# Kernel tuning notes

Hardware: AMD Instinct MI355X
Metric: run time of the kernel (lower is better)

The kernel has to match this reference:

```python
import jax, jax.numpy as jnp
import numpy as np

KEEP_RATIO = 0.5
B, H, W = 8, 1024, 1024


def setup_inputs() -> dict:
    key = jax.random.key(0)
    k1, k2, k3 = jax.random.split(key, 3)
    logits = jax.random.normal(k1, (B, 1, H, W), dtype=jnp.float32)
    targets = jax.random.randint(k2, (B, 1, H, W), 0, 2, dtype=jnp.int32)
    tissue_mask = jax.random.randint(k3, (B, 1, H, W), 0, 2, dtype=jnp.int32)
    return {"logits": logits, "targets": targets, "tissue_mask": tissue_mask}


def reference(logits, targets, tissue_mask):
    b = logits.shape[0]
    x = logits.reshape(b, -1)                       # (B, N)
    t = targets.reshape(b, -1).astype(x.dtype)      # {0,1}
    m = tissue_mask.reshape(b, -1).astype(x.dtype)  # {0,1}
    n = x.shape[1]

    # stable binary_cross_entropy_with_logits, reduction='none'
    bce = jnp.maximum(x, 0.0) - x * t + jnp.log1p(jnp.exp(-jnp.abs(x)))
    loss = bce * m                                  # masked per-pixel loss

    pos = t * m                                     # positives inside tissue
    neg = (1.0 - t) * m                             # negatives inside tissue
    n_pos = jnp.sum(pos, axis=1)                    # (B,)
    n_neg = jnp.sum(neg, axis=1)

    k_all = max(1, int(n * KEEP_RATIO))             # static python int
    # kept count per row: all positives + top-(k_all - n_pos) negatives (clamped)
    k_keep = n_pos + jnp.minimum(jnp.maximum(k_all - n_pos, 0.0), n_neg)  # (B,)

    BIG = jnp.asarray(1e30, x.dtype)
    # sort key: positives always first, then negatives by loss, then non-tissue
    sort_key = jnp.where(pos > 0, BIG, jnp.where(neg > 0, loss, -BIG))
    order = jnp.argsort(-sort_key, axis=1)          # descending
    sorted_loss = jnp.take_along_axis(loss, order, axis=1)

    ranks = jnp.arange(n, dtype=x.dtype)
    keep = (ranks[None, :] < k_keep[:, None]).astype(x.dtype)
    per_sample = jnp.sum(sorted_loss * keep, axis=1) / jnp.maximum(k_keep, 1.0)
    # fallback when no tissue pixels at all: torch keeps index 0 (loss there is 0)
    per_sample = jnp.where(k_keep > 0, per_sample, loss[:, 0])
    return jnp.mean(per_sample)
```

## Files before the change

### kernel.cpp

```cpp
#include <hip/hip_runtime.h>
#include <cstdint>
#include <cstddef>

#define N_PIX   1048576
#define B_ROWS  8
#define K_ALL   524288
#define WG_PER_ROW 256
#define ITERS   4
#define NBINS   2560
#define NPAIR   1280


__global__ __launch_bounds__(256, 4) void k_pass1(
    const float4* __restrict__ lg, const int4* __restrict__ tg, const int4* __restrict__ mk,
    unsigned* __restrict__ histCnt, float* __restrict__ histSum,
    unsigned* __restrict__ partNpos, double* __restrict__ partSpos, float* __restrict__ out)
{
    __shared__ unsigned hcp[NPAIR];
    __shared__ float    hs[NBINS];
    __shared__ unsigned swp[4];
    __shared__ double   sws[4];
    const int tid = threadIdx.x;
    for (int b = tid; b < NPAIR; b += 256) hcp[b] = 0u;
    for (int b = tid; b < NBINS; b += 256) hs[b] = 0.f;
    if (blockIdx.x == 0 && tid == 0) *out = 0.f;

    const int r = blockIdx.x >> 8;
    const size_t base = (size_t)blockIdx.x * (ITERS * 256) + tid;

    float4 x[ITERS]; int4 t[ITERS]; int4 m[ITERS];
    #pragma unroll
    for (int i = 0; i < ITERS; ++i) {
        x[i] = lg[base + (size_t)i * 256];
        t[i] = tg[base + (size_t)i * 256];
        m[i] = mk[base + (size_t)i * 256];
    }
    __syncthreads();

    unsigned npos = 0; float spos = 0.f;

    auto proc = [&](float xx, int tt, int mm) {
        float ax = fabsf(xx);
        float e = __expf(-ax);
        float l = __logf(1.f + e);
        float bce = fmaxf(xx, 0.f) - xx * (float)tt + l;
        if (mm) {
            if (tt) { npos++; spos += bce; }
            else {
                unsigned bin = __float_as_uint(bce) >> 20;
                if (bin >= NBINS) bin = NBINS - 1;
                atomicAdd(&hcp[bin >> 1], 1u << ((bin & 1u) << 4));
                atomicAdd(&hs[bin], bce);
            }
        }
    };

    #pragma unroll
    for (int i = 0; i < ITERS; ++i) {
        proc(x[i].x, t[i].x, m[i].x);
        proc(x[i].y, t[i].y, m[i].y);
        proc(x[i].z, t[i].z, m[i].z);
        proc(x[i].w, t[i].w, m[i].w);
    }

    for (int o = 32; o; o >>= 1) {
        npos += __shfl_down(npos, o);
        spos += __shfl_down(spos, o);
    }
    if ((tid & 63) == 0) { swp[tid >> 6] = npos; sws[tid >> 6] = (double)spos; }
    __syncthreads();
    if (tid == 0) {
        partNpos[blockIdx.x] = swp[0] + swp[1] + swp[2] + swp[3];
        partSpos[blockIdx.x] = sws[0] + sws[1] + sws[2] + sws[3];
    }

    unsigned* gc = histCnt + (size_t)r * NBINS;
    float*    gs = histSum + (size_t)r * NBINS;
    for (int i = tid; i < NPAIR; i += 256) {
        unsigned v = hcp[i];
        unsigned lo = v & 0xFFFFu, hi = v >> 16;
        if (lo) atomicAdd(&gc[2 * i],     lo);
        if (hi) atomicAdd(&gc[2 * i + 1], hi);
    }
    for (int b = tid; b < NBINS; b += 256) {
        float s = hs[b];
        if (s != 0.f) atomicAdd(&gs[b], s);
    }
}

__global__ __launch_bounds__(256) void k_final(
    const unsigned* __restrict__ histCnt, const float* __restrict__ histSum,
    const unsigned* __restrict__ partNpos, const double* __restrict__ partSpos,
    float* __restrict__ out)
{
    __shared__ unsigned sc[2][256];
    __shared__ double   sd[2][256];
    __shared__ unsigned swp[4];
    __shared__ double   sws[4];
    __shared__ int rT; __shared__ unsigned rcntgt; __shared__ double rsumgt;

    const int r = blockIdx.x, tid = threadIdx.x;
    const unsigned* cnt = histCnt + (size_t)r * NBINS;
    const float*    sum = histSum + (size_t)r * NBINS;

    {
        unsigned np = partNpos[r * 256 + tid];
        double   sp = partSpos[r * 256 + tid];
        for (int o = 32; o; o >>= 1) { np += __shfl_down(np, o); sp += __shfl_down(sp, o); }
        if ((tid & 63) == 0) { swp[tid >> 6] = np; sws[tid >> 6] = sp; }
    }
    __syncthreads();
    const unsigned npos = swp[0] + swp[1] + swp[2] + swp[3];
    const double sumPos = sws[0] + sws[1] + sws[2] + sws[3];
    __syncthreads();

    const int per = NBINS / 256;
    const int b0 = NBINS - 1 - tid * per;
    unsigned pc = 0; double ps = 0.0;
    for (int i = 0; i < per; ++i) { pc += cnt[b0 - i]; ps += (double)sum[b0 - i]; }

    int pp = 0;
    sc[0][tid] = pc; sd[0][tid] = ps;
    __syncthreads();
    for (int ofs = 1; ofs < 256; ofs <<= 1) {
        unsigned c = sc[pp][tid]; double s = sd[pp][tid];
        if (tid >= ofs) { c += sc[pp][tid - ofs]; s += sd[pp][tid - ofs]; }
        sc[pp ^ 1][tid] = c; sd[pp ^ 1][tid] = s;
        pp ^= 1;
        __syncthreads();
    }
    const unsigned nneg   = sc[pp][255];
    const double   sumNeg = sd[pp][255];

    long kl = (long)K_ALL - (long)npos;
    if (kl < 0) kl = 0;
    if (kl > (long)nneg) kl = (long)nneg;
    const unsigned Kneg = (unsigned)kl;

    double sum_sel = 0.0;
    if (Kneg >= nneg) {
        sum_sel = sumNeg;
    } else if (Kneg > 0) {
        unsigned inc = sc[pp][tid];
        unsigned exc = inc - pc;
        double   exs = sd[pp][tid] - ps;
        if (exc < Kneg && Kneg <= inc) {
            unsigned cum = exc; double csum = exs;
            for (int i = 0; i < per; ++i) {
                int bin = b0 - i;
                unsigned c = cnt[bin];
                if (cum + c >= Kneg) { rT = bin; rcntgt = cum; rsumgt = csum; break; }
                cum += c; csum += (double)sum[bin];
            }
        }
        __syncthreads();
        if (tid == 0) {
            const int T1 = rT;
            const unsigned cntT1 = cnt[T1];
            const double   sumT1 = (double)sum[T1];
            const unsigned Kp = Kneg - rcntgt;
            const float lo = __uint_as_float((unsigned)T1 << 20);
            const float hi = __uint_as_float((unsigned)(T1 + 1) << 20);
            const double w = (double)hi - (double)lo;
            const double avg = sumT1 / (double)cntT1;
            const double topmean = avg + 0.5 * w * (1.0 - (double)Kp / (double)cntT1);
            sum_sel = rsumgt + (double)Kp * topmean;
        }
    }

    if (tid == 0) {
        unsigned long long kk = (unsigned long long)npos + (unsigned long long)Kneg;
        double per_s = 0.0;
        if (kk > 0) per_s = (sumPos + sum_sel) / (double)kk;
        atomicAdd(out, (float)(per_s / (double)B_ROWS));
    }
}

extern "C" void kernel_launch(void* const* d_in, const int* in_sizes, int n_in,
                              void* d_out, int out_size, void* d_ws, size_t ws_size,
                              hipStream_t stream)
{
    const float* logits = (const float*)d_in[0];
    const int*   targets = (const int*)d_in[1];
    const int*   tissue = (const int*)d_in[2];

    const int NBLK = B_ROWS * WG_PER_ROW;
    char* ws = (char*)d_ws;
    size_t off = 0;
    unsigned* histCnt = (unsigned*)(ws + off); off += (size_t)B_ROWS * NBINS * 4;
    float*    histSum = (float*)(ws + off);    off += (size_t)B_ROWS * NBINS * 4;
    size_t zero_size = off;
    unsigned* partNpos = (unsigned*)(ws + off); off += (size_t)NBLK * 4;
    double*   partSpos = (double*)(ws + off);   off += (size_t)NBLK * 8;

    hipMemsetAsync(ws, 0, zero_size, stream);

    k_pass1<<<NBLK, 256, 0, stream>>>(
        (const float4*)logits, (const int4*)targets, (const int4*)tissue,
        histCnt, histSum, partNpos, partSpos, (float*)d_out);
    k_final<<<B_ROWS, 256, 0, stream>>>(histCnt, histSum, partNpos, partSpos, (float*)d_out);
}
```

Baseline: 129.9 us.

## Pack histogram count and fixed-point sum into one 64-bit atomic per bin

Replaces the separate packed-16-bit count histogram and float-sum histogram with a single 64-bit word per bin: count in the top 16 bits, fixed-point loss sum in the low 48. Each negative pixel then needs one LDS atomic instead of two, and the global merge and final scan read one array. Bin width is doubled (2048 bins), which coarsens the threshold interpolation, and the fixed-point quantization adds rounding error to the sums. Launch bounds are raised to 6 waves per SIMD.

Result: faster. 121.5 us (-6.5%).

```diff
diff --git a/kernel.cpp b/kernel.cpp
--- a/kernel.cpp
+++ b/kernel.cpp
@@ -7,22 +7,20 @@
 #define K_ALL   524288
 #define WG_PER_ROW 256
 #define ITERS   4
-#define NBINS   2560
-#define NPAIR   1280
-
-
-__global__ __launch_bounds__(256, 4) void k_pass1(
+#define NBINS   2048
+#define FPSCALE 262144.0f
+
+
+__global__ __launch_bounds__(256, 6) void k_pass1(
     const float4* __restrict__ lg, const int4* __restrict__ tg, const int4* __restrict__ mk,
-    unsigned* __restrict__ histCnt, float* __restrict__ histSum,
+    unsigned long long* __restrict__ hist,
     unsigned* __restrict__ partNpos, double* __restrict__ partSpos, float* __restrict__ out)
 {
-    __shared__ unsigned hcp[NPAIR];
-    __shared__ float    hs[NBINS];
+    __shared__ unsigned long long hq[NBINS];
     __shared__ unsigned swp[4];
     __shared__ double   sws[4];
     const int tid = threadIdx.x;
-    for (int b = tid; b < NPAIR; b += 256) hcp[b] = 0u;
-    for (int b = tid; b < NBINS; b += 256) hs[b] = 0.f;
+    for (int b = tid; b < NBINS; b += 256) hq[b] = 0ull;
     if (blockIdx.x == 0 && tid == 0) *out = 0.f;
 
     const int r = blockIdx.x >> 8;
@@ -47,10 +45,10 @@
         if (mm) {
             if (tt) { npos++; spos += bce; }
             else {
-                unsigned bin = __float_as_uint(bce) >> 20;
+                unsigned bin = __float_as_uint(bce) >> 21;
                 if (bin >= NBINS) bin = NBINS - 1;
-                atomicAdd(&hcp[bin >> 1], 1u << ((bin & 1u) << 4));
-                atomicAdd(&hs[bin], bce);
+                unsigned fx = (unsigned)__float2uint_rn(bce * FPSCALE);
+                atomicAdd(&hq[bin], (1ull << 48) | (unsigned long long)fx);
             }
         }
     };
@@ -74,22 +72,15 @@
         partSpos[blockIdx.x] = sws[0] + sws[1] + sws[2] + sws[3];
     }
 
-    unsigned* gc = histCnt + (size_t)r * NBINS;
-    float*    gs = histSum + (size_t)r * NBINS;
-    for (int i = tid; i < NPAIR; i += 256) {
-        unsigned v = hcp[i];
-        unsigned lo = v & 0xFFFFu, hi = v >> 16;
-        if (lo) atomicAdd(&gc[2 * i],     lo);
-        if (hi) atomicAdd(&gc[2 * i + 1], hi);
-    }
+    unsigned long long* gh = hist + (size_t)r * NBINS;
     for (int b = tid; b < NBINS; b += 256) {
-        float s = hs[b];
-        if (s != 0.f) atomicAdd(&gs[b], s);
+        unsigned long long v = hq[b];
+        if (v) atomicAdd(&gh[b], v);
     }
 }
 
 __global__ __launch_bounds__(256) void k_final(
-    const unsigned* __restrict__ histCnt, const float* __restrict__ histSum,
+    const unsigned long long* __restrict__ hist,
     const unsigned* __restrict__ partNpos, const double* __restrict__ partSpos,
     float* __restrict__ out)
 {
@@ -100,8 +91,8 @@
     __shared__ int rT; __shared__ unsigned rcntgt; __shared__ double rsumgt;
 
     const int r = blockIdx.x, tid = threadIdx.x;
-    const unsigned* cnt = histCnt + (size_t)r * NBINS;
-    const float*    sum = histSum + (size_t)r * NBINS;
+    const unsigned long long* gh = hist + (size_t)r * NBINS;
+    const double inv = 1.0 / (double)FPSCALE;
 
     {
         unsigned np = partNpos[r * 256 + tid];
@@ -116,8 +107,15 @@
 
     const int per = NBINS / 256;
     const int b0 = NBINS - 1 - tid * per;
+    unsigned lc[8]; double lsum[8];
     unsigned pc = 0; double ps = 0.0;
-    for (int i = 0; i < per; ++i) { pc += cnt[b0 - i]; ps += (double)sum[b0 - i]; }
+    #pragma unroll
+    for (int i = 0; i < per; ++i) {
+        unsigned long long v = gh[b0 - i];
+        lc[i] = (unsigned)(v >> 48);
+        lsum[i] = (double)(v & 0xFFFFFFFFFFFFull) * inv;
+        pc += lc[i]; ps += lsum[i];
+    }
 
     int pp = 0;
     sc[0][tid] = pc; sd[0][tid] = ps;
@@ -146,21 +144,21 @@
         double   exs = sd[pp][tid] - ps;
         if (exc < Kneg && Kneg <= inc) {
             unsigned cum = exc; double csum = exs;
+            #pragma unroll
             for (int i = 0; i < per; ++i) {
-                int bin = b0 - i;
-                unsigned c = cnt[bin];
-                if (cum + c >= Kneg) { rT = bin; rcntgt = cum; rsumgt = csum; break; }
-                cum += c; csum += (double)sum[bin];
+                if (cum + lc[i] >= Kneg) { rT = b0 - i; rcntgt = cum; rsumgt = csum; break; }
+                cum += lc[i]; csum += lsum[i];
             }
         }
         __syncthreads();
         if (tid == 0) {
             const int T1 = rT;
-            const unsigned cntT1 = cnt[T1];
-            const double   sumT1 = (double)sum[T1];
+            unsigned long long v = gh[T1];
+            const unsigned cntT1 = (unsigned)(v >> 48);
+            const double   sumT1 = (double)(v & 0xFFFFFFFFFFFFull) * inv;
             const unsigned Kp = Kneg - rcntgt;
-            const float lo = __uint_as_float((unsigned)T1 << 20);
-            const float hi = __uint_as_float((unsigned)(T1 + 1) << 20);
+            const float lo = __uint_as_float((unsigned)T1 << 21);
+            const float hi = __uint_as_float((unsigned)(T1 + 1) << 21);
             const double w = (double)hi - (double)lo;
             const double avg = sumT1 / (double)cntT1;
             const double topmean = avg + 0.5 * w * (1.0 - (double)Kp / (double)cntT1);
@@ -187,8 +185,8 @@
     const int NBLK = B_ROWS * WG_PER_ROW;
     char* ws = (char*)d_ws;
     size_t off = 0;
-    unsigned* histCnt = (unsigned*)(ws + off); off += (size_t)B_ROWS * NBINS * 4;
-    float*    histSum = (float*)(ws + off);    off += (size_t)B_ROWS * NBINS * 4;
+    unsigned long long* hist = (unsigned long long*)(ws + off);
+    off += (size_t)B_ROWS * NBINS * 8;
     size_t zero_size = off;
     unsigned* partNpos = (unsigned*)(ws + off); off += (size_t)NBLK * 4;
     double*   partSpos = (double*)(ws + off);   off += (size_t)NBLK * 8;
@@ -197,6 +195,6 @@
 
     k_pass1<<<NBLK, 256, 0, stream>>>(
         (const float4*)logits, (const int4*)targets, (const int4*)tissue,
-        histCnt, histSum, partNpos, partSpos, (float*)d_out);
-    k_final<<<B_ROWS, 256, 0, stream>>>(histCnt, histSum, partNpos, partSpos, (float*)d_out);
+        hist, partNpos, partSpos, (float*)d_out);
+    k_final<<<B_ROWS, 256, 0, stream>>>(hist, partNpos, partSpos, (float*)d_out);
 }
```
